# Kernel optimization log

Hardware: AMD Instinct MI355X
Metric: run time of the kernel (lower is better)

## Reference

```python
import jax, jax.numpy as jnp
import numpy as np

# module constants (match init_kwargs)
D_MODEL = 1024
N_HEADS = 16
D_K = 64
CHUNK_LEN = 64
EPS = 1e-8

B, C, N, NL = 4, 16, 2, 128  # batch, chunks, neighbors, neighbor_len
S = C * CHUNK_LEN            # seq_len = 1024


def setup_inputs() -> dict:
    key = jax.random.key(0)
    ks = jax.random.split(key, 10)
    s = 0.02
    HD = N_HEADS * D_K
    return {
        "h": jax.random.normal(ks[0], (B, S, D_MODEL), jnp.float32),
        "e": jax.random.normal(ks[1], (B, C, N, NL, D_MODEL), jnp.float32),
        "g_norm": jnp.ones((D_MODEL,), jnp.float32),
        "Wq": jax.random.normal(ks[2], (D_MODEL, HD), jnp.float32) * s,
        "bq": jnp.zeros((HD,), jnp.float32),
        "Wk": jax.random.normal(ks[3], (D_MODEL, HD), jnp.float32) * s,
        "bk": jnp.zeros((HD,), jnp.float32),
        "Wv": jax.random.normal(ks[4], (D_MODEL, HD), jnp.float32) * s,
        "bv": jnp.zeros((HD,), jnp.float32),
        "Wo": jax.random.normal(ks[5], (HD, D_MODEL), jnp.float32) * s,
        "bo": jnp.zeros((D_MODEL,), jnp.float32),
    }


def _rmsnorm(x, g):
    return x * g * jax.lax.rsqrt(jnp.mean(x * x, axis=-1, keepdims=True) + EPS)


def reference(h, e, g_norm, Wq, bq, Wk, bk, Wv, bv, Wo, bo):
    b, seq, d = h.shape
    _, c, n, nl, _ = e.shape
    cl = CHUNK_LEN
    scale = 1.0 / np.sqrt(D_K).astype(np.float32)

    h_res = h
    hn = _rmsnorm(h[:, cl - 1:], g_norm)                 # [b, seq-cl+1, d]
    pad = c * cl - hn.shape[1]
    hn = jnp.pad(hn, ((0, 0), (0, pad), (0, 0)))         # [b, c*cl, d]
    hn = hn.reshape(b, c, cl, d)

    q = (hn @ Wq + bq).reshape(b, c, cl, N_HEADS, D_K)       # bcihd
    k = (e @ Wk + bk).reshape(b, c, n, nl, N_HEADS, D_K)     # bcnjhd
    v = (e @ Wv + bv).reshape(b, c, n, nl, N_HEADS, D_K)

    attn = jnp.einsum('bcihd,bcnjhd->bchinj', q, k) * scale  # [b,c,h,i,n,j]
    attn = jax.nn.softmax(attn.reshape(b, c, N_HEADS, cl, n * nl), axis=-1)
    attn = attn.reshape(b, c, N_HEADS, cl, n, nl)

    o = jnp.einsum('bchinj,bcnjhd->bcihd', attn, v)
    o = o.reshape(b, c * cl, N_HEADS * D_K)
    o = o @ Wo + bo                                          # [b, c*cl, d]
    o = jnp.pad(o, ((0, 0), (cl - 1, 0), (0, 0)))            # shift right by cl-1
    return o[:, :seq] + h_res
```

## Files before the change

### kernel.cpp

```cpp
#include <hip/hip_runtime.h>
#include <stdint.h>

#define DEV __device__ __forceinline__

typedef __attribute__((ext_vector_type(8))) __bf16 bf16x8;
typedef __attribute__((ext_vector_type(4))) float floatx4;

DEV float bf2f(unsigned short u) {
  union { unsigned int i; float f; } x; x.i = ((unsigned int)u) << 16; return x.f;
}
DEV unsigned int f2bf(float f) {
  union { float f; unsigned int i; } x; x.f = f;
  unsigned int r = x.i + 0x7FFFu + ((x.i >> 16) & 1u);
  return r >> 16;
}
DEV void gl2lds16(const unsigned short* g, unsigned short* l) {
  __builtin_amdgcn_global_load_lds(
      (const __attribute__((address_space(1))) unsigned int*)g,
      (__attribute__((address_space(3))) unsigned int*)l, 16, 0, 0);
}
DEV floatx4 zero4() { floatx4 z; z[0]=0.f; z[1]=0.f; z[2]=0.f; z[3]=0.f; return z; }

__global__ void cca_transpose_k(const float* __restrict__ W0,
                                const float* __restrict__ W1,
                                const float* __restrict__ W2,
                                const float* __restrict__ W3,
                                unsigned short* __restrict__ D0,
                                unsigned short* __restrict__ D1,
                                unsigned short* __restrict__ D2,
                                unsigned short* __restrict__ D3) {
  __shared__ float tile[64][65];
  const float* W; unsigned short* Wt;
  switch (blockIdx.z) {
    case 0: W = W0; Wt = D0; break;
    case 1: W = W1; Wt = D1; break;
    case 2: W = W2; Wt = D2; break;
    default: W = W3; Wt = D3; break;
  }
  const int K = 1024, N = 1024;
  int k0 = blockIdx.x * 64, n0 = blockIdx.y * 64;
  int t = threadIdx.x;
  int c = t & 63, r4 = t >> 6;
#pragma unroll
  for (int it = 0; it < 16; ++it) {
    int r = it * 4 + r4;
    tile[r][c] = W[(size_t)(k0 + r) * N + n0 + c];
  }
  __syncthreads();
#pragma unroll
  for (int it = 0; it < 16; ++it) {
    int r = it * 4 + r4;
    Wt[(size_t)(n0 + r) * K + k0 + c] = (unsigned short)f2bf(tile[c][r]);
  }
}

__global__ void cca_prep_k(const float* __restrict__ e,
                           unsigned short* __restrict__ eb,
                           const float* __restrict__ h,
                           const float* __restrict__ g,
                           unsigned short* __restrict__ hn,
                           float* __restrict__ out) {
  int blk = blockIdx.x;
  int t = threadIdx.x;
  if (blk < 16384) {
    int i = blk * 256 + t;
    float4 v = ((const float4*)e)[i];
    uint2 o;
    o.x = f2bf(v.x) | (f2bf(v.y) << 16);
    o.y = f2bf(v.z) | (f2bf(v.w) << 16);
    ((uint2*)eb)[i] = o;
    return;
  }
  if (blk < 20480) {
    int row = blk - 16384;
    int b = row >> 10, p = row & 1023;
    unsigned short* dst = hn + (size_t)row * 1024;
    if (p >= 961) {
      uint2 z; z.x = 0u; z.y = 0u;
      ((uint2*)dst)[t] = z;
      return;
    }
    const float* src = h + ((size_t)(b << 10) + p + 63) * 1024;
    float4 v = ((const float4*)src)[t];
    float ss = v.x*v.x + v.y*v.y + v.z*v.z + v.w*v.w;
#pragma unroll
    for (int m = 32; m > 0; m >>= 1) ss += __shfl_down(ss, m);
    __shared__ float wsum[4];
    int lane = t & 63, wv = t >> 6;
    if (lane == 0) wsum[wv] = ss;
    __syncthreads();
    float tot = wsum[0] + wsum[1] + wsum[2] + wsum[3];
    float r = rsqrtf(tot * (1.0f / 1024.0f) + 1e-8f);
    float4 gv = ((const float4*)g)[t];
    uint2 outp;
    outp.x = f2bf(v.x * gv.x * r) | (f2bf(v.y * gv.y * r) << 16);
    outp.y = f2bf(v.z * gv.z * r) | (f2bf(v.w * gv.w * r) << 16);
    ((uint2*)dst)[t] = outp;
    return;
  }
  {
    int idx = (blk - 20480) * 256 + t;
    const int n4 = 4 * 63 * 1024 / 4;
    if (idx < n4) {
      int e4 = idx * 4;
      int b = e4 / (63 * 1024);
      int r = e4 - b * (63 * 1024);
      size_t off = (size_t)b * 1024 * 1024 + (size_t)r;
      *(float4*)(out + off) = *(const float4*)(h + off);
    }
  }
}

template <int MODE>
__launch_bounds__(256, 2)
__global__ void cca_gemm_k(const unsigned short* __restrict__ A,
                           const unsigned short* __restrict__ Bt,
                           const float* __restrict__ bias1,
                           const float* __restrict__ bias2,
                           const float* __restrict__ resid,
                           void* __restrict__ Cout,
                           int M, int N, int K) {
  __shared__ unsigned short Ash[128 * 32];
  __shared__ unsigned short Bsh[128 * 32];
  int tM = blockIdx.x * 128, tN = blockIdx.y * 128;
  int t = threadIdx.x, lane = t & 63, wv = t >> 6;
  int wm = wv >> 1, wn = wv & 1;
  int l15 = lane & 15, quad = lane >> 4;
  int arow = lane >> 2, achk = lane & 3;
  int gchk = achk ^ ((arow >> 1) & 3);
  int rchk = quad ^ ((l15 >> 1) & 3);
  floatx4 acc[4][4];
#pragma unroll
  for (int i = 0; i < 4; ++i)
#pragma unroll
    for (int j = 0; j < 4; ++j) acc[i][j] = zero4();

  for (int k0 = 0; k0 < K; k0 += 32) {
    __syncthreads();
#pragma unroll
    for (int ii = 0; ii < 2; ++ii) {
      int seg = wv + ii * 4;
      int row = seg * 16 + arow;
      gl2lds16(A + (size_t)(tM + row) * K + k0 + gchk * 8, Ash + seg * 512);
      gl2lds16(Bt + (size_t)(tN + row) * K + k0 + gchk * 8, Bsh + seg * 512);
    }
    __syncthreads();
    bf16x8 af[4], bfv[4];
#pragma unroll
    for (int mt = 0; mt < 4; ++mt)
      af[mt] = *(const bf16x8*)&Ash[(wm * 64 + mt * 16 + l15) * 32 + rchk * 8];
#pragma unroll
    for (int nt = 0; nt < 4; ++nt)
      bfv[nt] = *(const bf16x8*)&Bsh[(wn * 64 + nt * 16 + l15) * 32 + rchk * 8];
#pragma unroll
    for (int mt = 0; mt < 4; ++mt)
#pragma unroll
      for (int nt = 0; nt < 4; ++nt)
        acc[mt][nt] = __builtin_amdgcn_mfma_f32_16x16x32_bf16(af[mt], bfv[nt], acc[mt][nt], 0, 0, 0);
  }

#pragma unroll
  for (int mt = 0; mt < 4; ++mt) {
    int mrow = tM + wm * 64 + mt * 16 + quad * 4;
#pragma unroll
    for (int nt = 0; nt < 4; ++nt) {
      int ncol = tN + wn * 64 + nt * 16 + l15;
      float bs;
      if (MODE == 0) {
        bs = (bias2 != nullptr && ncol >= 1024) ? bias2[ncol - 1024] : bias1[ncol];
      } else {
        bs = bias1[ncol];
      }
#pragma unroll
      for (int r = 0; r < 4; ++r) {
        int m = mrow + r;
        float v = acc[mt][nt][r] + bs;
        if (MODE == 0) {
          ((unsigned short*)Cout)[(size_t)m * N + ncol] = (unsigned short)f2bf(v);
        } else {
          int p = m & 1023;
          if (p < 961) {
            size_t o = (size_t)(m + 63) * 1024 + (size_t)ncol;
            ((float*)Cout)[o] = v + resid[o];
          }
        }
      }
    }
  }
}

__launch_bounds__(256, 2)
__global__ void cca_attn_k(const unsigned short* __restrict__ Q,
                           const unsigned short* __restrict__ KV,
                           unsigned short* __restrict__ O) {
  __shared__ unsigned short smemA[64 * 64 + 256 * 64];
  __shared__ unsigned short VT[64 * 264];
  unsigned short* Qsh = smemA;
  unsigned short* Ksh = smemA + 64 * 64;
  unsigned short* Psh = smemA;
  int bch = blockIdx.x;
  int hh = bch & 15, c = (bch >> 4) & 15, b = bch >> 8;
  int t = threadIdx.x, lane = t & 63, wv = t >> 6;
  int l15 = lane & 15, quad = lane >> 4;
  size_t qbase = (size_t)b * 1024 + (size_t)c * 64;
  size_t kvbase = (size_t)b * 4096 + (size_t)c * 256;
  int hoff = hh * 64;

  {
    int rowi = lane >> 3, chk = lane & 7;
#pragma unroll
    for (int ii = 0; ii < 2; ++ii) {
      int seg = wv + ii * 4;
      int row = seg * 8 + rowi;
      gl2lds16(Q + (qbase + row) * 1024 + hoff + chk * 8, Qsh + seg * 512);
    }
#pragma unroll
    for (int ii = 0; ii < 8; ++ii) {
      int seg = wv + ii * 4;
      int row = seg * 8 + rowi;
      gl2lds16(KV + (kvbase + row) * 2048 + hoff + chk * 8, Ksh + seg * 512);
    }
  }
  {
    const unsigned short* vp = KV + (kvbase + t) * 2048 + 1024 + hoff;
#pragma unroll
    for (int d0 = 0; d0 < 64; d0 += 8) {
      uint4 raw = *(const uint4*)(vp + d0);
      unsigned int w0 = raw.x, w1 = raw.y, w2 = raw.z, w3 = raw.w;
      VT[(d0 + 0) * 264 + t] = (unsigned short)(w0 & 0xffff);
      VT[(d0 + 1) * 264 + t] = (unsigned short)(w0 >> 16);
      VT[(d0 + 2) * 264 + t] = (unsigned short)(w1 & 0xffff);
      VT[(d0 + 3) * 264 + t] = (unsigned short)(w1 >> 16);
      VT[(d0 + 4) * 264 + t] = (unsigned short)(w2 & 0xffff);
      VT[(d0 + 5) * 264 + t] = (unsigned short)(w2 >> 16);
      VT[(d0 + 6) * 264 + t] = (unsigned short)(w3 & 0xffff);
      VT[(d0 + 7) * 264 + t] = (unsigned short)(w3 >> 16);
    }
  }
  __syncthreads();

  floatx4 st[16];
#pragma unroll
  for (int i = 0; i < 16; ++i) st[i] = zero4();
  bf16x8 a0 = *(const bf16x8*)&Qsh[(wv * 16 + l15) * 64 + quad * 8];
  bf16x8 a1 = *(const bf16x8*)&Qsh[(wv * 16 + l15) * 64 + 32 + quad * 8];
#pragma unroll
  for (int kt = 0; kt < 16; ++kt) {
    bf16x8 b0 = *(const bf16x8*)&Ksh[(kt * 16 + l15) * 64 + quad * 8];
    bf16x8 b1 = *(const bf16x8*)&Ksh[(kt * 16 + l15) * 64 + 32 + quad * 8];
    st[kt] = __builtin_amdgcn_mfma_f32_16x16x32_bf16(a0, b0, st[kt], 0, 0, 0);
    st[kt] = __builtin_amdgcn_mfma_f32_16x16x32_bf16(a1, b1, st[kt], 0, 0, 0);
  }
  __syncthreads();

  const float scale = 0.125f;
#pragma unroll
  for (int r = 0; r < 4; ++r) {
    float mx = -1e30f;
#pragma unroll
    for (int kt = 0; kt < 16; ++kt) mx = fmaxf(mx, st[kt][r]);
    mx = fmaxf(mx, __shfl_xor(mx, 1));
    mx = fmaxf(mx, __shfl_xor(mx, 2));
    mx = fmaxf(mx, __shfl_xor(mx, 4));
    mx = fmaxf(mx, __shfl_xor(mx, 8));
    float sum = 0.f;
#pragma unroll
    for (int kt = 0; kt < 16; ++kt) {
      float e = __expf((st[kt][r] - mx) * scale);
      st[kt][r] = e;
      sum += e;
    }
    sum += __shfl_xor(sum, 1);
    sum += __shfl_xor(sum, 2);
    sum += __shfl_xor(sum, 4);
    sum += __shfl_xor(sum, 8);
    float inv = 1.0f / sum;
    int prow = wv * 16 + quad * 4 + r;
#pragma unroll
    for (int kt = 0; kt < 16; ++kt)
      Psh[prow * 264 + kt * 16 + l15] = (unsigned short)f2bf(st[kt][r] * inv);
  }

  floatx4 ot[4];
#pragma unroll
  for (int nt = 0; nt < 4; ++nt) ot[nt] = zero4();
#pragma unroll
  for (int kt2 = 0; kt2 < 8; ++kt2) {
    bf16x8 ap = *(const bf16x8*)&Psh[(wv * 16 + l15) * 264 + kt2 * 32 + quad * 8];
#pragma unroll
    for (int nt = 0; nt < 4; ++nt) {
      bf16x8 bv8 = *(const bf16x8*)&VT[(nt * 16 + l15) * 264 + kt2 * 32 + quad * 8];
      ot[nt] = __builtin_amdgcn_mfma_f32_16x16x32_bf16(ap, bv8, ot[nt], 0, 0, 0);
    }
  }
#pragma unroll
  for (int nt = 0; nt < 4; ++nt) {
#pragma unroll
    for (int r = 0; r < 4; ++r) {
      int i = wv * 16 + quad * 4 + r;
      int dcol = hoff + nt * 16 + l15;
      O[(qbase + i) * 1024 + dcol] = (unsigned short)f2bf(ot[nt][r]);
    }
  }
}

extern "C" void kernel_launch(void* const* d_in, const int* in_sizes, int n_in,
                              void* d_out, int out_size, void* d_ws, size_t ws_size,
                              hipStream_t stream) {
  const float* h  = (const float*)d_in[0];
  const float* e  = (const float*)d_in[1];
  const float* g  = (const float*)d_in[2];
  const float* Wq = (const float*)d_in[3];
  const float* bq = (const float*)d_in[4];
  const float* Wk = (const float*)d_in[5];
  const float* bk = (const float*)d_in[6];
  const float* Wv = (const float*)d_in[7];
  const float* bv = (const float*)d_in[8];
  const float* Wo = (const float*)d_in[9];
  const float* bo = (const float*)d_in[10];
  float* out = (float*)d_out;

  unsigned short* ws   = (unsigned short*)d_ws;
  unsigned short* hn   = ws;
  unsigned short* WqT  = hn   + (size_t)4096 * 1024;
  unsigned short* WkvT = WqT  + (size_t)1024 * 1024;
  unsigned short* WoT  = WkvT + (size_t)2048 * 1024;
  unsigned short* Qb   = WoT  + (size_t)1024 * 1024;
  unsigned short* KVb  = Qb   + (size_t)4096 * 1024;
  unsigned short* Ob   = KVb  + (size_t)16384 * 2048;
  unsigned short* eb   = Ob   + (size_t)4096 * 1024;

  cca_transpose_k<<<dim3(16, 16, 4), 256, 0, stream>>>(
      Wq, Wk, Wv, Wo, WqT, WkvT, WkvT + (size_t)1024 * 1024, WoT);

  cca_prep_k<<<20732, 256, 0, stream>>>(e, eb, h, g, hn, out);

  cca_gemm_k<0><<<dim3(32, 8), 256, 0, stream>>>(hn, WqT, bq, nullptr, nullptr,
                                                 (void*)Qb, 4096, 1024, 1024);
  cca_gemm_k<0><<<dim3(128, 16), 256, 0, stream>>>(eb, WkvT, bk, bv, nullptr,
                                                   (void*)KVb, 16384, 2048, 1024);

  cca_attn_k<<<1024, 256, 0, stream>>>(Qb, KVb, Ob);

  cca_gemm_k<1><<<dim3(32, 8), 256, 0, stream>>>(Ob, WoT, bo, nullptr, h,
                                                 (void*)out, 4096, 1024, 1024);
}
```

Before: 308.7 us.

## Pre-transpose V into swizzled global buffer and async-load it in attention

Adds a separate kernel that transposes each (batch, chunk, head) V tile into an XOR-swizzled layout in a scratch buffer that reuses the e-bf16 workspace. The attention kernel then loads V with async global-to-LDS copies instead of doing scalar 16-bit transposed LDS stores, and reads it back with a swizzled index to avoid bank conflicts. This costs an extra kernel launch and an extra global round trip for V, in exchange for cheaper staging inside the attention kernel.

```diff
diff --git a/kernel.cpp b/kernel.cpp
--- a/kernel.cpp
+++ b/kernel.cpp
@@ -189,12 +189,49 @@
   }
 }
 
+__global__ void cca_vt_k(const unsigned short* __restrict__ KV,
+                         unsigned short* __restrict__ VTb) {
+  __shared__ unsigned short tile[256 * 66];
+  int bch = blockIdx.x;
+  int hh = bch & 15, c = (bch >> 4) & 15, b = bch >> 8;
+  size_t kvbase = (size_t)b * 4096 + (size_t)c * 256;
+  int t = threadIdx.x;
+#pragma unroll
+  for (int it = 0; it < 16; ++it) {
+    int flat = it * 256 + t;
+    int row = flat >> 4, cu = flat & 15;
+    uint2 v = *(const uint2*)(KV + (kvbase + row) * 2048 + 1024 + hh * 64 + cu * 4);
+    int d0 = cu * 4;
+    tile[row * 66 + d0 + 0] = (unsigned short)(v.x & 0xffff);
+    tile[row * 66 + d0 + 1] = (unsigned short)(v.x >> 16);
+    tile[row * 66 + d0 + 2] = (unsigned short)(v.y & 0xffff);
+    tile[row * 66 + d0 + 3] = (unsigned short)(v.y >> 16);
+  }
+  __syncthreads();
+  unsigned short* dst = VTb + (size_t)bch * 16384;
+#pragma unroll
+  for (int it = 0; it < 16; ++it) {
+    int flat = it * 256 + t;
+    int d = flat >> 6, ju = flat & 63;
+    int j = ju * 4;
+    unsigned int lo = (unsigned int)tile[(j + 0) * 66 + d] |
+                      ((unsigned int)tile[(j + 1) * 66 + d] << 16);
+    unsigned int hi = (unsigned int)tile[(j + 2) * 66 + d] |
+                      ((unsigned int)tile[(j + 3) * 66 + d] << 16);
+    int u = j >> 3, joff = j & 7;
+    int phys = d * 256 + ((u ^ (d & 7)) << 3) + joff;
+    uint2 o; o.x = lo; o.y = hi;
+    *(uint2*)(dst + phys) = o;
+  }
+}
+
 __launch_bounds__(256, 2)
 __global__ void cca_attn_k(const unsigned short* __restrict__ Q,
                            const unsigned short* __restrict__ KV,
+                           const unsigned short* __restrict__ VTb,
                            unsigned short* __restrict__ O) {
   __shared__ unsigned short smemA[64 * 64 + 256 * 64];
-  __shared__ unsigned short VT[64 * 264];
+  __shared__ unsigned short VTlds[64 * 256];
   unsigned short* Qsh = smemA;
   unsigned short* Ksh = smemA + 64 * 64;
   unsigned short* Psh = smemA;
@@ -220,21 +257,11 @@
       int row = seg * 8 + rowi;
       gl2lds16(KV + (kvbase + row) * 2048 + hoff + chk * 8, Ksh + seg * 512);
     }
-  }
-  {
-    const unsigned short* vp = KV + (kvbase + t) * 2048 + 1024 + hoff;
-#pragma unroll
-    for (int d0 = 0; d0 < 64; d0 += 8) {
-      uint4 raw = *(const uint4*)(vp + d0);
-      unsigned int w0 = raw.x, w1 = raw.y, w2 = raw.z, w3 = raw.w;
-      VT[(d0 + 0) * 264 + t] = (unsigned short)(w0 & 0xffff);
-      VT[(d0 + 1) * 264 + t] = (unsigned short)(w0 >> 16);
-      VT[(d0 + 2) * 264 + t] = (unsigned short)(w1 & 0xffff);
-      VT[(d0 + 3) * 264 + t] = (unsigned short)(w1 >> 16);
-      VT[(d0 + 4) * 264 + t] = (unsigned short)(w2 & 0xffff);
-      VT[(d0 + 5) * 264 + t] = (unsigned short)(w2 >> 16);
-      VT[(d0 + 6) * 264 + t] = (unsigned short)(w3 & 0xffff);
-      VT[(d0 + 7) * 264 + t] = (unsigned short)(w3 >> 16);
+    const unsigned short* vsrc = VTb + (size_t)bch * 16384;
+#pragma unroll
+    for (int ii = 0; ii < 8; ++ii) {
+      int seg = wv + ii * 4;
+      gl2lds16(vsrc + seg * 512 + lane * 8, VTlds + seg * 512);
     }
   }
   __syncthreads();
@@ -289,7 +316,9 @@
     bf16x8 ap = *(const bf16x8*)&Psh[(wv * 16 + l15) * 264 + kt2 * 32 + quad * 8];
 #pragma unroll
     for (int nt = 0; nt < 4; ++nt) {
-      bf16x8 bv8 = *(const bf16x8*)&VT[(nt * 16 + l15) * 264 + kt2 * 32 + quad * 8];
+      int vrow = nt * 16 + l15;
+      int u = kt2 * 4 + quad;
+      bf16x8 bv8 = *(const bf16x8*)&VTlds[vrow * 256 + ((u ^ (vrow & 7)) << 3)];
       ot[nt] = __builtin_amdgcn_mfma_f32_16x16x32_bf16(ap, bv8, ot[nt], 0, 0, 0);
     }
   }
@@ -329,6 +358,7 @@
   unsigned short* KVb  = Qb   + (size_t)4096 * 1024;
   unsigned short* Ob   = KVb  + (size_t)16384 * 2048;
   unsigned short* eb   = Ob   + (size_t)4096 * 1024;
+  unsigned short* VTb  = eb;
 
   cca_transpose_k<<<dim3(16, 16, 4), 256, 0, stream>>>(
       Wq, Wk, Wv, Wo, WqT, WkvT, WkvT + (size_t)1024 * 1024, WoT);
@@ -340,7 +370,9 @@
   cca_gemm_k<0><<<dim3(128, 16), 256, 0, stream>>>(eb, WkvT, bk, bv, nullptr,
                                                    (void*)KVb, 16384, 2048, 1024);
 
-  cca_attn_k<<<1024, 256, 0, stream>>>(Qb, KVb, Ob);
+  cca_vt_k<<<1024, 256, 0, stream>>>(KVb, VTb);
+
+  cca_attn_k<<<1024, 256, 0, stream>>>(Qb, KVb, VTb, Ob);
 
   cca_gemm_k<1><<<dim3(32, 8), 256, 0, stream>>>(Ob, WoT, bo, nullptr, h,
                                                  (void*)out, 4096, 1024, 1024);
```

Measured after the change: 313.0 us. Within noise of the previous version (+1.4%).
